# Performance work log

Hardware: AMD Instinct MI355X
Metric: run time of the kernel (lower is better)

## Reference

```python
import jax, jax.numpy as jnp
import numpy as np

BSZ, N_VARS, IN_DIM, OUT_DIM, N_CLUSTER = 128, 321, 336, 96, 8


def setup_inputs() -> dict:
    key = jax.random.key(0)
    k1, k2, k3, k4 = jax.random.split(key, 4)
    x = jax.random.normal(k1, (BSZ, N_VARS, IN_DIM), dtype=jnp.float32)
    prob = jax.random.uniform(k2, (BSZ, N_VARS, N_CLUSTER), dtype=jnp.float32)
    # per-cluster Linear params, stacked: W[c] is (out_dim, in_dim), b[c] is (out_dim,)
    bound = 1.0 / np.sqrt(IN_DIM)
    W = jax.random.uniform(k3, (N_CLUSTER, OUT_DIM, IN_DIM), minval=-bound, maxval=bound, dtype=jnp.float32)
    b = jax.random.uniform(k4, (N_CLUSTER, OUT_DIM), minval=-bound, maxval=bound, dtype=jnp.float32)
    return {"x": x, "prob": prob, "W": W, "b": b}


def reference(x, prob, W, b):
    # Original: for each cluster c, y_c = x @ W[c].T + b[c]  -> stack (b,v,out,c)
    # then matmul with prob (b,v,c,1) -> prob-weighted combine over clusters.
    # Fused: combine cluster weighting inline, never materializing the stack.
    # x: (b, v, i); W: (c, o, i); prob: (b, v, c) -> out: (b, v, o)
    out = jnp.einsum('bvi,coi,bvc->bvo', x, W, prob)
    out = out + jnp.einsum('bvc,co->bvo', prob, b)
    return out
```

## Files before the change

kernel.cpp:

```cpp
#include <hip/hip_runtime.h>

#define BSZ 128
#define NV 321
#define IN_DIM 336
#define OUT_DIM 96
#define NC 8
#define ROWS (BSZ * NV)
#define KSTEPS 11
#define NCH (NC * KSTEPS)
#define CHUNK_HALFS 3072
#define CHUNK_BYTES 6144
#define NRING 8

typedef _Float16 half8 __attribute__((ext_vector_type(8)));
typedef float floatx4 __attribute__((ext_vector_type(4)));
typedef float floatx2 __attribute__((ext_vector_type(2)));

__global__ __launch_bounds__(256) void convert_w_kernel(
    const float* __restrict__ W, const float* __restrict__ b,
    _Float16* __restrict__ w16p) {
  int t = blockIdx.x * 256 + threadIdx.x;
  if (t >= NCH * OUT_DIM * 4) return;
  int lg = t & 3;
  int o = (t >> 2) % OUT_DIM;
  int chunk = (t >> 2) / OUT_DIM;
  int ks = chunk % KSTEPS;
  int c = chunk / KSTEPS;
  int k0 = ks * 32 + lg * 8;
  const float* wr = W + (size_t)(c * OUT_DIM + o) * IN_DIM;
  half8 h;
#pragma unroll
  for (int j = 0; j < 8; ++j) {
    int k = k0 + j;
    float v = (k < IN_DIM) ? wr[k] : ((k == IN_DIM) ? b[c * OUT_DIM + o] : 0.0f);
    h[j] = (_Float16)v;
  }
  *(half8*)(w16p + (size_t)chunk * CHUNK_HALFS + lg * 768 + o * 8) = h;
}

__device__ __forceinline__ void stage16(const _Float16* g, const _Float16* l) {
  __builtin_amdgcn_global_load_lds(
      (const __attribute__((address_space(1))) void*)g,
      (__attribute__((address_space(3))) void*)l, 16, 0, 0);
}

__device__ __forceinline__ half8 cvt8(floatx4 f0, floatx4 f1) {
  half8 h;
  h[0] = (_Float16)f0[0]; h[1] = (_Float16)f0[1];
  h[2] = (_Float16)f0[2]; h[3] = (_Float16)f0[3];
  h[4] = (_Float16)f1[0]; h[5] = (_Float16)f1[1];
  h[6] = (_Float16)f1[2]; h[7] = (_Float16)f1[3];
  return h;
}

__global__ __launch_bounds__(256, 2) void cluster_gemm_kernel(
    const float* __restrict__ x, const float* __restrict__ prob,
    const _Float16* __restrict__ w16p, float* __restrict__ out) {
  __shared__ __align__(16) _Float16 bb[NRING][CHUNK_HALFS];
  __shared__ float probs[64 * NC];

  const int tid = threadIdx.x;
  const int rbase = blockIdx.x * 64;
  const int lane = tid & 63;
  const int wave = tid >> 6;
  const int wm = wave >> 1;
  const int wc = wave & 1;
  const int l15 = lane & 15;
  const int lg = lane >> 4;

  {
    floatx2 v = *(const floatx2*)(prob + (size_t)rbase * NC + tid * 2);
    *(floatx2*)&probs[tid * 2] = v;
  }

  half8 a[2][KSTEPS];
#pragma unroll
  for (int m = 0; m < 2; ++m) {
    const float* xr = x + (size_t)(rbase + wm * 32 + m * 16 + l15) * IN_DIM + lg * 8;
#pragma unroll
    for (int ks = 0; ks < 10; ++ks) {
      floatx4 f0 = *(const floatx4*)(xr + ks * 32);
      floatx4 f1 = *(const floatx4*)(xr + ks * 32 + 4);
      a[m][ks] = cvt8(f0, f1);
    }
    if (lg < 2) {
      floatx4 f0 = *(const floatx4*)(xr + 320);
      floatx4 f1 = *(const floatx4*)(xr + 320 + 4);
      a[m][10] = cvt8(f0, f1);
    } else {
      half8 z = {};
      if (lg == 2) z[0] = (_Float16)1.0f;
      a[m][10] = z;
    }
  }

  asm volatile("s_waitcnt vmcnt(0)" ::: "memory");

  const int seg0 = (wave < 2) ? wave * 2048 : 4096 + (wave - 2) * 1024;
  const int nseg = (wave < 2) ? 2 : 1;
  const int lane16 = lane * 16;

#define STAGE(CH)                                                              \
  do {                                                                         \
    const char* gsrc = (const char*)(w16p + (size_t)(CH) * CHUNK_HALFS);       \
    char* ldst = (char*)&bb[(CH) & (NRING - 1)][0];                            \
    stage16((const _Float16*)(gsrc + seg0 + lane16),                           \
            (const _Float16*)(ldst + seg0));                                   \
    if (nseg == 2)                                                             \
      stage16((const _Float16*)(gsrc + seg0 + 1024 + lane16),                  \
              (const _Float16*)(ldst + seg0 + 1024));                          \
  } while (0)

  STAGE(0); STAGE(1); STAGE(2); STAGE(3); STAGE(4); STAGE(5); STAGE(6);

  if (wave < 2) asm volatile("s_waitcnt vmcnt(12)" ::: "memory");
  else          asm volatile("s_waitcnt vmcnt(6)" ::: "memory");
  asm volatile("s_waitcnt lgkmcnt(0)" ::: "memory");
  __builtin_amdgcn_s_barrier();

  const int rdoff = lg * 768 + (wc * 48 + l15) * 8;

  half8 bcur0 = *(const half8*)(&bb[0][rdoff]);
  half8 bcur1 = *(const half8*)(&bb[0][rdoff + 128]);
  half8 bcur2 = *(const half8*)(&bb[0][rdoff + 256]);

  floatx4 oacc[2][3] = {};
  floatx4 acc[2][3] = {};

  for (int c = 0; c < NC; ++c) {
#pragma unroll
    for (int ks = 0; ks < KSTEPS; ++ks) {
      const int it = c * KSTEPS + ks;

      if (wave < 2) asm volatile("s_waitcnt vmcnt(10)" ::: "memory");
      else          asm volatile("s_waitcnt vmcnt(5)" ::: "memory");
      __builtin_amdgcn_s_barrier();

      if (it + 7 < NCH) STAGE(it + 7);

      half8 bn0 = {}, bn1 = {}, bn2 = {};
      if (it + 1 < NCH) {
        const _Float16* bp = &bb[(it + 1) & (NRING - 1)][rdoff];
        bn0 = *(const half8*)(bp);
        bn1 = *(const half8*)(bp + 128);
        bn2 = *(const half8*)(bp + 256);
      }

      acc[0][0] = __builtin_amdgcn_mfma_f32_16x16x32_f16(a[0][ks], bcur0, acc[0][0], 0, 0, 0);
      acc[1][0] = __builtin_amdgcn_mfma_f32_16x16x32_f16(a[1][ks], bcur0, acc[1][0], 0, 0, 0);
      acc[0][1] = __builtin_amdgcn_mfma_f32_16x16x32_f16(a[0][ks], bcur1, acc[0][1], 0, 0, 0);
      acc[1][1] = __builtin_amdgcn_mfma_f32_16x16x32_f16(a[1][ks], bcur1, acc[1][1], 0, 0, 0);
      acc[0][2] = __builtin_amdgcn_mfma_f32_16x16x32_f16(a[0][ks], bcur2, acc[0][2], 0, 0, 0);
      acc[1][2] = __builtin_amdgcn_mfma_f32_16x16x32_f16(a[1][ks], bcur2, acc[1][2], 0, 0, 0);

      if (ks == KSTEPS - 1) {
#pragma unroll
        for (int m = 0; m < 2; ++m) {
#pragma unroll
          for (int r = 0; r < 4; ++r) {
            float p = probs[(wm * 32 + m * 16 + lg * 4 + r) * NC + c];
            oacc[m][0][r] += p * acc[m][0][r];
            oacc[m][1][r] += p * acc[m][1][r];
            oacc[m][2][r] += p * acc[m][2][r];
          }
          acc[m][0] = (floatx4){0.f, 0.f, 0.f, 0.f};
          acc[m][1] = (floatx4){0.f, 0.f, 0.f, 0.f};
          acc[m][2] = (floatx4){0.f, 0.f, 0.f, 0.f};
        }
      }

      bcur0 = bn0; bcur1 = bn1; bcur2 = bn2;
    }
  }

#pragma unroll
  for (int m = 0; m < 2; ++m) {
#pragma unroll
    for (int n = 0; n < 3; ++n) {
#pragma unroll
      for (int r = 0; r < 4; ++r) {
        int grow = rbase + wm * 32 + m * 16 + lg * 4 + r;
        out[(size_t)grow * OUT_DIM + wc * 48 + n * 16 + l15] = oacc[m][n][r];
      }
    }
  }
#undef STAGE
}

extern "C" void kernel_launch(void* const* d_in, const int* in_sizes, int n_in,
                              void* d_out, int out_size, void* d_ws, size_t ws_size,
                              hipStream_t stream) {
  const float* x = (const float*)d_in[0];
  const float* prob = (const float*)d_in[1];
  const float* W = (const float*)d_in[2];
  const float* b = (const float*)d_in[3];
  float* out = (float*)d_out;
  _Float16* w16p = (_Float16*)d_ws;

  const int ct = NCH * OUT_DIM * 4;
  hipLaunchKernelGGL(convert_w_kernel, dim3((ct + 255) / 256), dim3(256), 0,
                     stream, W, b, w16p);
  hipLaunchKernelGGL(cluster_gemm_kernel, dim3(ROWS / 64), dim3(256), 0, stream,
                     x, prob, w16p, out);
}
```

Before: 147.9 us.

## Replace LDS-staged weight ring with direct global-to-register prefetch pipeline

Removes the shared-memory ring buffer filled by global_load_lds and the per-iteration workgroup barriers. Each wave now loads its weight fragments straight from global (L2-resident) memory into a 5-deep register ring, using a vmcnt wait instead of barriers. This cuts LDS traffic and barrier synchronisation, but duplicates weight fetches across waves and raises register pressure from the fully unrolled 88-iteration loop.

```diff
diff --git a/kernel.cpp b/kernel.cpp
--- a/kernel.cpp
+++ b/kernel.cpp
@@ -9,8 +9,7 @@
 #define KSTEPS 11
 #define NCH (NC * KSTEPS)
 #define CHUNK_HALFS 3072
-#define CHUNK_BYTES 6144
-#define NRING 8
+#define DPTH 5
 
 typedef _Float16 half8 __attribute__((ext_vector_type(8)));
 typedef float floatx4 __attribute__((ext_vector_type(4)));
@@ -38,12 +37,6 @@
   *(half8*)(w16p + (size_t)chunk * CHUNK_HALFS + lg * 768 + o * 8) = h;
 }
 
-__device__ __forceinline__ void stage16(const _Float16* g, const _Float16* l) {
-  __builtin_amdgcn_global_load_lds(
-      (const __attribute__((address_space(1))) void*)g,
-      (__attribute__((address_space(3))) void*)l, 16, 0, 0);
-}
-
 __device__ __forceinline__ half8 cvt8(floatx4 f0, floatx4 f1) {
   half8 h;
   h[0] = (_Float16)f0[0]; h[1] = (_Float16)f0[1];
@@ -56,7 +49,6 @@
 __global__ __launch_bounds__(256, 2) void cluster_gemm_kernel(
     const float* __restrict__ x, const float* __restrict__ prob,
     const _Float16* __restrict__ w16p, float* __restrict__ out) {
-  __shared__ __align__(16) _Float16 bb[NRING][CHUNK_HALFS];
   __shared__ float probs[64 * NC];
 
   const int tid = threadIdx.x;
@@ -94,83 +86,59 @@
     }
   }
 
-  asm volatile("s_waitcnt vmcnt(0)" ::: "memory");
+  asm volatile("s_waitcnt vmcnt(0) lgkmcnt(0)" ::: "memory");
+  __syncthreads();
 
-  const int seg0 = (wave < 2) ? wave * 2048 : 4096 + (wave - 2) * 1024;
-  const int nseg = (wave < 2) ? 2 : 1;
-  const int lane16 = lane * 16;
+  const _Float16* bq = w16p + lg * 768 + (wc * 48 + l15) * 8;
 
-#define STAGE(CH)                                                              \
-  do {                                                                         \
-    const char* gsrc = (const char*)(w16p + (size_t)(CH) * CHUNK_HALFS);       \
-    char* ldst = (char*)&bb[(CH) & (NRING - 1)][0];                            \
-    stage16((const _Float16*)(gsrc + seg0 + lane16),                           \
-            (const _Float16*)(ldst + seg0));                                   \
-    if (nseg == 2)                                                             \
-      stage16((const _Float16*)(gsrc + seg0 + 1024 + lane16),                  \
-              (const _Float16*)(ldst + seg0 + 1024));                          \
-  } while (0)
-
-  STAGE(0); STAGE(1); STAGE(2); STAGE(3); STAGE(4); STAGE(5); STAGE(6);
-
-  if (wave < 2) asm volatile("s_waitcnt vmcnt(12)" ::: "memory");
-  else          asm volatile("s_waitcnt vmcnt(6)" ::: "memory");
-  asm volatile("s_waitcnt lgkmcnt(0)" ::: "memory");
-  __builtin_amdgcn_s_barrier();
-
-  const int rdoff = lg * 768 + (wc * 48 + l15) * 8;
-
-  half8 bcur0 = *(const half8*)(&bb[0][rdoff]);
-  half8 bcur1 = *(const half8*)(&bb[0][rdoff + 128]);
-  half8 bcur2 = *(const half8*)(&bb[0][rdoff + 256]);
+  half8 ring[DPTH][3];
+#pragma unroll
+  for (int p = 0; p < DPTH; ++p) {
+    ring[p][0] = *(const half8*)(bq + p * CHUNK_HALFS);
+    ring[p][1] = *(const half8*)(bq + p * CHUNK_HALFS + 128);
+    ring[p][2] = *(const half8*)(bq + p * CHUNK_HALFS + 256);
+  }
 
   floatx4 oacc[2][3] = {};
   floatx4 acc[2][3] = {};
 
-  for (int c = 0; c < NC; ++c) {
 #pragma unroll
-    for (int ks = 0; ks < KSTEPS; ++ks) {
-      const int it = c * KSTEPS + ks;
+  for (int it = 0; it < NCH; ++it) {
+    const int ks = it % KSTEPS;
+    const int c = it / KSTEPS;
+    const int slot = it % DPTH;
 
-      if (wave < 2) asm volatile("s_waitcnt vmcnt(10)" ::: "memory");
-      else          asm volatile("s_waitcnt vmcnt(5)" ::: "memory");
-      __builtin_amdgcn_s_barrier();
+    const int pc = (it + DPTH < NCH) ? (it + DPTH) : (NCH - 1);
+    half8 n0 = *(const half8*)(bq + pc * CHUNK_HALFS);
+    half8 n1 = *(const half8*)(bq + pc * CHUNK_HALFS + 128);
+    half8 n2 = *(const half8*)(bq + pc * CHUNK_HALFS + 256);
 
-      if (it + 7 < NCH) STAGE(it + 7);
+    asm volatile("s_waitcnt vmcnt(15)" ::: "memory");
 
-      half8 bn0 = {}, bn1 = {}, bn2 = {};
-      if (it + 1 < NCH) {
-        const _Float16* bp = &bb[(it + 1) & (NRING - 1)][rdoff];
-        bn0 = *(const half8*)(bp);
-        bn1 = *(const half8*)(bp + 128);
-        bn2 = *(const half8*)(bp + 256);
+    acc[0][0] = __builtin_amdgcn_mfma_f32_16x16x32_f16(a[0][ks], ring[slot][0], acc[0][0], 0, 0, 0);
+    acc[1][0] = __builtin_amdgcn_mfma_f32_16x16x32_f16(a[1][ks], ring[slot][0], acc[1][0], 0, 0, 0);
+    acc[0][1] = __builtin_amdgcn_mfma_f32_16x16x32_f16(a[0][ks], ring[slot][1], acc[0][1], 0, 0, 0);
+    acc[1][1] = __builtin_amdgcn_mfma_f32_16x16x32_f16(a[1][ks], ring[slot][1], acc[1][1], 0, 0, 0);
+    acc[0][2] = __builtin_amdgcn_mfma_f32_16x16x32_f16(a[0][ks], ring[slot][2], acc[0][2], 0, 0, 0);
+    acc[1][2] = __builtin_amdgcn_mfma_f32_16x16x32_f16(a[1][ks], ring[slot][2], acc[1][2], 0, 0, 0);
+
+    if (ks == KSTEPS - 1) {
+#pragma unroll
+      for (int m = 0; m < 2; ++m) {
+#pragma unroll
+        for (int r = 0; r < 4; ++r) {
+          float p = probs[(wm * 32 + m * 16 + lg * 4 + r) * NC + c];
+          oacc[m][0][r] += p * acc[m][0][r];
+          oacc[m][1][r] += p * acc[m][1][r];
+          oacc[m][2][r] += p * acc[m][2][r];
+        }
+        acc[m][0] = (floatx4){0.f, 0.f, 0.f, 0.f};
+        acc[m][1] = (floatx4){0.f, 0.f, 0.f, 0.f};
+        acc[m][2] = (floatx4){0.f, 0.f, 0.f, 0.f};
       }
+    }
 
-      acc[0][0] = __builtin_amdgcn_mfma_f32_16x16x32_f16(a[0][ks], bcur0, acc[0][0], 0, 0, 0);
-      acc[1][0] = __builtin_amdgcn_mfma_f32_16x16x32_f16(a[1][ks], bcur0, acc[1][0], 0, 0, 0);
-      acc[0][1] = __builtin_amdgcn_mfma_f32_16x16x32_f16(a[0][ks], bcur1, acc[0][1], 0, 0, 0);
-      acc[1][1] = __builtin_amdgcn_mfma_f32_16x16x32_f16(a[1][ks], bcur1, acc[1][1], 0, 0, 0);
-      acc[0][2] = __builtin_amdgcn_mfma_f32_16x16x32_f16(a[0][ks], bcur2, acc[0][2], 0, 0, 0);
-      acc[1][2] = __builtin_amdgcn_mfma_f32_16x16x32_f16(a[1][ks], bcur2, acc[1][2], 0, 0, 0);
-
-      if (ks == KSTEPS - 1) {
-#pragma unroll
-        for (int m = 0; m < 2; ++m) {
-#pragma unroll
-          for (int r = 0; r < 4; ++r) {
-            float p = probs[(wm * 32 + m * 16 + lg * 4 + r) * NC + c];
-            oacc[m][0][r] += p * acc[m][0][r];
-            oacc[m][1][r] += p * acc[m][1][r];
-            oacc[m][2][r] += p * acc[m][2][r];
-          }
-          acc[m][0] = (floatx4){0.f, 0.f, 0.f, 0.f};
-          acc[m][1] = (floatx4){0.f, 0.f, 0.f, 0.f};
-          acc[m][2] = (floatx4){0.f, 0.f, 0.f, 0.f};
-        }
-      }
-
-      bcur0 = bn0; bcur1 = bn1; bcur2 = bn2;
-    }
+    ring[slot][0] = n0; ring[slot][1] = n1; ring[slot][2] = n2;
   }
 
 #pragma unroll
@@ -184,7 +152,6 @@
       }
     }
   }
-#undef STAGE
 }
 
 extern "C" void kernel_launch(void* const* d_in, const int* in_sizes, int n_in,
```

After: 218.8 us. 47.9% more time.
